# Kernel tuning notes

Hardware: AMD Instinct MI355X
Metric: run time of the kernel (lower is better)

Reference implementation:

```python
import jax, jax.numpy as jnp
import numpy as np

B, IN, H0, H1, OUT = 4096, 1024, 4096, 4096, 1024
QMAX = 127.0


def setup_inputs() -> dict:
    key = jax.random.key(0)
    k0, k1, k2, k3 = jax.random.split(key, 4)
    x = jax.random.normal(k0, (B, IN), dtype=jnp.float32)
    # Linear weights hold already-quantized integer values (module casts .int())
    W0 = jax.random.randint(k1, (H0, IN + 1), -127, 128).astype(jnp.int32)
    W1 = jax.random.randint(k2, (H1, H0 + 1), -127, 128).astype(jnp.int32)
    W2 = jax.random.randint(k3, (OUT, H1 + 1), -127, 128).astype(jnp.int32)
    return {
        "x": x,
        "a_in0": jnp.float32(4.0), "a_w0": jnp.float32(0.05),
        "a_in2": jnp.float32(50.0), "a_w2": jnp.float32(0.05),
        "a_in4": jnp.float32(50.0), "a_w4": jnp.float32(0.05),
        "W0": W0, "W1": W1, "W2": W2,
    }


def _quant(x, amax):
    # clamp(round(x * 127/amax), -127, 127) -> int32
    return jnp.clip(jnp.round(x * (QMAX / amax)), -QMAX, QMAX).astype(jnp.int32)


def _qlinear(x, W, a_in, a_w):
    q = _quant(x, a_in)                                   # [B, K] int32
    ones = jnp.ones((q.shape[0], 1), dtype=jnp.int32)     # folded bias column
    q = jnp.concatenate([q, ones], axis=1)                # [B, K+1]
    acc = q @ W.T                                         # int32 GEMM [B, N]
    return acc.astype(jnp.float32) * (a_w * a_in / (QMAX * QMAX))


def reference(x, a_in0, a_w0, a_in2, a_w2, a_in4, a_w4, W0, W1, W2):
    x = x.reshape(x.shape[0], -1)
    x = _qlinear(x, W0, a_in0, a_w0)
    x = jax.nn.relu(x)
    x = _qlinear(x, W1, a_in2, a_w2)
    x = jax.nn.relu(x)
    x = _qlinear(x, W2, a_in4, a_w4)
    return x
```

## Files before the change

### kernel.cpp

```cpp
#include <hip/hip_runtime.h>

#define QMAX 127.0f

typedef int v4i __attribute__((ext_vector_type(4)));

__device__ __forceinline__ void gload_lds16(const void* g, void* l) {
  __builtin_amdgcn_global_load_lds(
      (const __attribute__((address_space(1))) void*)g,
      (__attribute__((address_space(3))) void*)l, 16, 0, 0);
}

__device__ __forceinline__ void pack_body(const int* __restrict__ W,
                                          signed char* __restrict__ W8,
                                          int* __restrict__ bias,
                                          unsigned lblk, int kshift) {
  unsigned t = lblk * 256u + threadIdx.x;
  unsigned row = t >> kshift;
  unsigned j = t & ((1u << kshift) - 1u);
  unsigned K = 4u << kshift;
  size_t srcBase = (size_t)row * (size_t)(K + 1) + (size_t)j * 4;
  int c0 = W[srcBase + 0], c1 = W[srcBase + 1], c2 = W[srcBase + 2], c3 = W[srcBase + 3];
  unsigned packed = (unsigned)(c0 & 0xff) | ((unsigned)(c1 & 0xff) << 8) |
                    ((unsigned)(c2 & 0xff) << 16) | ((unsigned)(c3 & 0xff) << 24);
  reinterpret_cast<unsigned*>(W8)[t] = packed;
  if (j == 0) bias[row] = W[(size_t)row * (K + 1) + K];
}

__global__ void prep_kernel(const float* __restrict__ x,
                            signed char* __restrict__ qa0,
                            const float* __restrict__ pAin,
                            const int* __restrict__ W0, signed char* __restrict__ W0p, int* __restrict__ b0,
                            const int* __restrict__ W1, signed char* __restrict__ W1p, int* __restrict__ b1,
                            const int* __restrict__ W2, signed char* __restrict__ W2p, int* __restrict__ b2) {
  unsigned blk = blockIdx.x;
  if (blk < 4096u) {
    pack_body(W0, W0p, b0, blk, 8);
  } else if (blk < 20480u) {
    pack_body(W1, W1p, b1, blk - 4096u, 10);
  } else if (blk < 24576u) {
    pack_body(W2, W2p, b2, blk - 20480u, 10);
  } else {
    unsigned t = (blk - 24576u) * 256u + threadIdx.x;
    float s = QMAX / pAin[0];
    float4 v = reinterpret_cast<const float4*>(x)[t];
    int q0 = (int)fminf(fmaxf(rintf(v.x * s), -QMAX), QMAX);
    int q1 = (int)fminf(fmaxf(rintf(v.y * s), -QMAX), QMAX);
    int q2 = (int)fminf(fmaxf(rintf(v.z * s), -QMAX), QMAX);
    int q3 = (int)fminf(fmaxf(rintf(v.w * s), -QMAX), QMAX);
    unsigned packed = (unsigned)(q0 & 0xff) | ((unsigned)(q1 & 0xff) << 8) |
                      ((unsigned)(q2 & 0xff) << 16) | ((unsigned)(q3 & 0xff) << 24);
    reinterpret_cast<unsigned*>(qa0)[t] = packed;
  }
}


#define FENCE() asm volatile("" ::: "memory")
#define BARRIER()                      \
  do {                                 \
    FENCE();                           \
    __builtin_amdgcn_s_barrier();      \
    FENCE();                           \
  } while (0)
#define LGK0() asm volatile("s_waitcnt lgkmcnt(0)" ::: "memory")
#define VMC6() asm volatile("s_waitcnt vmcnt(6)" ::: "memory")
#define VMC0() asm volatile("s_waitcnt vmcnt(0)" ::: "memory")

#define STAGE_A(bf, h, t)                                                     \
  do {                                                                        \
    const signed char* _g = gA + (size_t)((h) * 128) * K + (size_t)(t) * 128; \
    signed char* _l = ldsA + (bf) * 32768 + (h) * 16384 + ldsThr;             \
    gload_lds16(_g, _l);                                                      \
    gload_lds16(_g + (size_t)8 * K, _l + 1024);                               \
  } while (0)

#define STAGE_B(bf, h, t)                                                     \
  do {                                                                        \
    const signed char* _g = gB + (size_t)((h) * 128) * K + (size_t)(t) * 128; \
    signed char* _l = ldsB + (bf) * 32768 + (h) * 16384 + ldsThr;             \
    gload_lds16(_g, _l);                                                      \
    gload_lds16(_g + (size_t)8 * K, _l + 1024);                               \
  } while (0)

#define LDAQ(bf, qm, kk, dst)                                                 \
  do {                                                                        \
    _Pragma("unroll") for (int m = 0; m < 4; ++m) {                           \
      int row = wm * 128 + (qm) * 64 + m * 16 + l15;                          \
      int off = ((kk) * 64 + hi * 16) ^ ((row & 7) << 4);                     \
      dst[m] = *(const v4i*)(ldsA + (bf) * 32768 + row * 128 + off);          \
    }                                                                         \
  } while (0)

#define LDBH(bf, kk)                                                          \
  do {                                                                        \
    _Pragma("unroll") for (int n = 0; n < 4; ++n) {                           \
      int row = wn * 64 + n * 16 + l15;                                       \
      int off = ((kk) * 64 + hi * 16) ^ ((row & 7) << 4);                     \
      bR[n][kk] = *(const v4i*)(ldsB + (bf) * 32768 + row * 128 + off);       \
    }                                                                         \
  } while (0)

#define MFMAQK(qm, kk, asrc)                                                  \
  do {                                                                        \
    __builtin_amdgcn_s_setprio(1);                                            \
    _Pragma("unroll") for (int m = 0; m < 4; ++m)                             \
    _Pragma("unroll") for (int n = 0; n < 4; ++n)                             \
      acc[(qm) * 4 + m][n] = __builtin_amdgcn_mfma_i32_16x16x64_i8(           \
          asrc[m], bR[n][kk], acc[(qm) * 4 + m][n], 0, 0, 0);                 \
    __builtin_amdgcn_s_setprio(0);                                            \
  } while (0)

__global__ __launch_bounds__(512, 2)
void qgemm256_kernel(const signed char* __restrict__ A,
                     const signed char* __restrict__ Bw,
                     const int* __restrict__ bias,
                     signed char* __restrict__ O,
                     int N, int K, int nbn,
                     const float* __restrict__ pAin,
                     const float* __restrict__ pAw,
                     const float* __restrict__ pAnext) {
  extern __shared__ signed char lds[];
  signed char* ldsA = lds;
  signed char* ldsB = lds + 65536;

  const int nwg = gridDim.x, bid = blockIdx.x, per = nwg >> 3;
  const int swz = (bid & 7) * per + (bid >> 3);
  const int brow = swz / nbn, bcol = swz - brow * nbn;
  const int browBase = brow << 8, bcolBase = bcol << 8;

  const int tid = threadIdx.x;
  const int lane = tid & 63, l15 = lane & 15, hi = lane >> 4;
  const int wid = tid >> 6, wm = wid >> 2, wn = wid & 3;

  const int rloc = (wid << 4) + (lane >> 3);
  const int csrc = (lane & 7) ^ ((lane >> 3) & 7);
  const signed char* gA = A + (size_t)(browBase + rloc) * K + csrc * 16;
  const signed char* gB = Bw + (size_t)(bcolBase + rloc) * K + csrc * 16;
  const int ldsThr = (wid << 11) + lane * 16;

  v4i acc[8][4] = {};
  v4i bR[4][2];

  const int nk = K >> 7, niter = nk >> 1, nkm = nk - 1;

  STAGE_B(0, 0, 0); STAGE_B(0, 1, 0); STAGE_A(0, 0, 0); STAGE_A(0, 1, 0);
  STAGE_B(1, 0, 1); STAGE_B(1, 1, 1); STAGE_A(1, 0, 1);
  VMC6();
  BARRIER();

#pragma unroll 1
  for (int i = 0; i < niter; ++i) {
    const int t1 = 2 * i + 1;
    const int tE = (2 * i + 2) & nkm;
    const int tO = (2 * i + 3) & nkm;
    v4i a00[4], a01[4], a10[4], a11[4];
    LDAQ(0, 0, 0, a00); LDBH(0, 0); LDAQ(0, 0, 1, a01); LDBH(0, 1);
    STAGE_A(1, 1, t1);
    BARRIER();
    MFMAQK(0, 0, a00);
    LGK0();
    BARRIER();
    LDAQ(0, 1, 0, a10);
    STAGE_B(0, 0, tE);
    BARRIER();
    MFMAQK(0, 1, a01);
    BARRIER();
    LDAQ(0, 1, 1, a11);
    STAGE_B(0, 1, tE);
    BARRIER();
    MFMAQK(1, 0, a10);
    LGK0();
    BARRIER();
    STAGE_A(0, 0, tE);
    VMC6();
    BARRIER();
    MFMAQK(1, 1, a11);
    BARRIER();
    LDAQ(1, 0, 0, a00); LDBH(1, 0); LDAQ(1, 0, 1, a01); LDBH(1, 1);
    STAGE_A(0, 1, tE);
    BARRIER();
    MFMAQK(0, 0, a00);
    LGK0();
    BARRIER();
    LDAQ(1, 1, 0, a10);
    STAGE_B(1, 0, tO);
    BARRIER();
    MFMAQK(0, 1, a01);
    BARRIER();
    LDAQ(1, 1, 1, a11);
    STAGE_B(1, 1, tO);
    BARRIER();
    MFMAQK(1, 0, a10);
    LGK0();
    BARRIER();
    STAGE_A(1, 0, tO);
    VMC6();
    BARRIER();
    MFMAQK(1, 1, a11);
    BARRIER();
  }

  VMC0();

  const float sDeq = (pAw[0] * pAin[0]) / (QMAX * QMAX);
  const float sQ = QMAX / pAnext[0];
#pragma unroll
  for (int nf = 0; nf < 4; ++nf) {
    const int gcol = bcolBase + wn * 64 + nf * 16 + l15;
    const int bv = bias[gcol];
#pragma unroll
    for (int mf = 0; mf < 8; ++mf) {
      const int gr = browBase + wm * 128 + mf * 16 + (hi << 2);
#pragma unroll
      for (int r = 0; r < 4; ++r) {
        float f = (float)(acc[mf][nf][r] + bv) * sDeq;
        f = fmaxf(f, 0.0f);
        float qf = fminf(fmaxf(rintf(f * sQ), -QMAX), QMAX);
        O[(size_t)(gr + r) * N + gcol] = (signed char)(int)qf;
      }
    }
  }
}

__global__ __launch_bounds__(256)
void qgemm_kernel(const signed char* __restrict__ A,
                  const signed char* __restrict__ Bw,
                  const int* __restrict__ bias,
                  float* __restrict__ O,
                  int N, int K, int nbn,
                  const float* __restrict__ pAin,
                  const float* __restrict__ pAw) {
  __shared__ signed char slds[32768];
  signed char* ldsA = slds;
  signed char* ldsB = slds + 16384;

  int nwg = gridDim.x;
  int bid = blockIdx.x;
  int per = nwg >> 3;
  int swz = (bid & 7) * per + (bid >> 3);
  int brow = swz / nbn;
  int bcol = swz - brow * nbn;
  int browBase = brow << 7;
  int bcolBase = bcol << 7;

  int tid = threadIdx.x;
  int lane = tid & 63;
  int l15 = lane & 15;
  int hi = lane >> 4;
  int wid = tid >> 6;
  int wr = (wid >> 1) << 6;
  int wc = (wid & 1) << 6;

  v4i acc[4][4] = {};

  int nk = K >> 7;
  for (int kt = 0; kt < nk; ++kt) {
    int k0 = kt << 7;
#pragma unroll
    for (int i = 0; i < 4; ++i) {
      int c = i * 256 + tid;
      int r = c >> 3;
      int osrc = ((c & 7) << 4) ^ ((r & 7) << 4);
      gload_lds16(A + (size_t)(browBase + r) * K + (k0 + osrc), ldsA + c * 16);
      gload_lds16(Bw + (size_t)(bcolBase + r) * K + (k0 + osrc), ldsB + c * 16);
    }
    __syncthreads();
#pragma unroll
    for (int kk = 0; kk < 2; ++kk) {
      v4i a[4], b[4];
#pragma unroll
      for (int m = 0; m < 4; ++m) {
        int row = wr + m * 16 + l15;
        int off = (kk * 64 + hi * 16) ^ ((row & 7) << 4);
        a[m] = *reinterpret_cast<const v4i*>(ldsA + row * 128 + off);
      }
#pragma unroll
      for (int n = 0; n < 4; ++n) {
        int row = wc + n * 16 + l15;
        int off = (kk * 64 + hi * 16) ^ ((row & 7) << 4);
        b[n] = *reinterpret_cast<const v4i*>(ldsB + row * 128 + off);
      }
#pragma unroll
      for (int m = 0; m < 4; ++m)
#pragma unroll
        for (int n = 0; n < 4; ++n)
          acc[m][n] = __builtin_amdgcn_mfma_i32_16x16x64_i8(a[m], b[n], acc[m][n], 0, 0, 0);
    }
    __syncthreads();
  }

  float sDeq = (pAw[0] * pAin[0]) / (QMAX * QMAX);
#pragma unroll
  for (int n = 0; n < 4; ++n) {
    int gcol = bcolBase + wc + n * 16 + l15;
    int bv = bias[gcol];
#pragma unroll
    for (int m = 0; m < 4; ++m) {
      int growb = browBase + wr + m * 16 + (hi << 2);
#pragma unroll
      for (int r = 0; r < 4; ++r) {
        O[(size_t)(growb + r) * N + gcol] = (float)(acc[m][n][r] + bv) * sDeq;
      }
    }
  }
}

extern "C" void kernel_launch(void* const* d_in, const int* in_sizes, int n_in,
                              void* d_out, int out_size, void* d_ws, size_t ws_size,
                              hipStream_t stream) {
  const float* x     = (const float*)d_in[0];
  const float* a_in0 = (const float*)d_in[1];
  const float* a_w0  = (const float*)d_in[2];
  const float* a_in2 = (const float*)d_in[3];
  const float* a_w2  = (const float*)d_in[4];
  const float* a_in4 = (const float*)d_in[5];
  const float* a_w4  = (const float*)d_in[6];
  const int*   W0    = (const int*)d_in[7];
  const int*   W1    = (const int*)d_in[8];
  const int*   W2    = (const int*)d_in[9];
  float* out = (float*)d_out;

  constexpr int B = 4096, IN = 1024, H0 = 4096, H1 = 4096, OUTN = 1024;

  char* ws = (char*)d_ws;
  size_t off = 0;
  auto alloc = [&](size_t sz) {
    char* p = ws + off;
    off += (sz + 255) & ~(size_t)255;
    return p;
  };
  signed char* qa0 = (signed char*)alloc((size_t)B * IN);
  signed char* qa1 = (signed char*)alloc((size_t)B * H0);
  signed char* qa2 = (signed char*)alloc((size_t)B * H1);
  signed char* W0p = (signed char*)alloc((size_t)H0 * IN);
  signed char* W1p = (signed char*)alloc((size_t)H1 * H0);
  signed char* W2p = (signed char*)alloc((size_t)OUTN * H1);
  int* b0 = (int*)alloc((size_t)H0 * 4);
  int* b1 = (int*)alloc((size_t)H1 * 4);
  int* b2 = (int*)alloc((size_t)OUTN * 4);

  hipFuncSetAttribute((const void*)qgemm256_kernel,
                      hipFuncAttributeMaxDynamicSharedMemorySize, 131072);

  prep_kernel<<<28672, 256, 0, stream>>>(x, qa0, a_in0,
                                         W0, W0p, b0,
                                         W1, W1p, b1,
                                         W2, W2p, b2);

  qgemm256_kernel<<<(B / 256) * (H0 / 256), 512, 131072, stream>>>(
      qa0, W0p, b0, qa1, H0, IN, H0 / 256, a_in0, a_w0, a_in2);

  qgemm256_kernel<<<(B / 256) * (H1 / 256), 512, 131072, stream>>>(
      qa1, W1p, b1, qa2, H1, H0, H1 / 256, a_in2, a_w2, a_in4);

  qgemm_kernel<<<(B / 128) * (OUTN / 128), 256, 0, stream>>>(
      qa2, W2p, b2, out, OUTN, H1, OUTN / 128, a_in4, a_w4);
}
```

Measured before the change: 141.5 us.

## Switch 256-tile int8 GEMM to 32x32x32 MFMA with prefetched LDS fragments

Replaces the 16x16x64 i8 MFMA tiles in the 256x256 kernel with 32x32x32 i8 MFMAs on a 4x2 fragment grid per wave. The K-loop is restructured so that LDS reads for the next 32-wide k-chunk are issued before the MFMAs of the current chunk, using ping-pong A registers. The goal is fewer LDS reads per MFMA and better overlap of LDS latency with matrix math. The cost is a more complex epilogue row mapping and higher register pressure from the 16-wide accumulators.

Measured after the change: 150.3 us. 1.06x slower.

```diff
diff --git a/kernel.cpp b/kernel.cpp
--- a/kernel.cpp
+++ b/kernel.cpp
@@ -3,6 +3,7 @@
 #define QMAX 127.0f
 
 typedef int v4i __attribute__((ext_vector_type(4)));
+typedef int v16i __attribute__((ext_vector_type(16)));
 
 __device__ __forceinline__ void gload_lds16(const void* g, void* l) {
   __builtin_amdgcn_global_load_lds(
@@ -81,31 +82,31 @@
     gload_lds16(_g + (size_t)8 * K, _l + 1024);                               \
   } while (0)
 
-#define LDAQ(bf, qm, kk, dst)                                                 \
-  do {                                                                        \
-    _Pragma("unroll") for (int m = 0; m < 4; ++m) {                           \
-      int row = wm * 128 + (qm) * 64 + m * 16 + l15;                          \
-      int off = ((kk) * 64 + hi * 16) ^ ((row & 7) << 4);                     \
-      dst[m] = *(const v4i*)(ldsA + (bf) * 32768 + row * 128 + off);          \
+#define LDA4(bf, kc, dst)                                                     \
+  do {                                                                        \
+    _Pragma("unroll") for (int mf = 0; mf < 4; ++mf) {                        \
+      int row = wm * 128 + mf * 32 + l31;                                     \
+      int off = ((kc) * 32 + hk * 16) ^ ((row & 7) << 4);                     \
+      dst[mf] = *(const v4i*)(ldsA + (bf) * 32768 + row * 128 + off);         \
     }                                                                         \
   } while (0)
 
-#define LDBH(bf, kk)                                                          \
-  do {                                                                        \
-    _Pragma("unroll") for (int n = 0; n < 4; ++n) {                           \
-      int row = wn * 64 + n * 16 + l15;                                       \
-      int off = ((kk) * 64 + hi * 16) ^ ((row & 7) << 4);                     \
-      bR[n][kk] = *(const v4i*)(ldsB + (bf) * 32768 + row * 128 + off);       \
+#define LDB2(bf, kc)                                                          \
+  do {                                                                        \
+    _Pragma("unroll") for (int nf = 0; nf < 2; ++nf) {                        \
+      int row = wn * 64 + nf * 32 + l31;                                      \
+      int off = ((kc) * 32 + hk * 16) ^ ((row & 7) << 4);                     \
+      bF[nf][kc] = *(const v4i*)(ldsB + (bf) * 32768 + row * 128 + off);      \
     }                                                                         \
   } while (0)
 
-#define MFMAQK(qm, kk, asrc)                                                  \
+#define MFMA8(aset, kc)                                                       \
   do {                                                                        \
     __builtin_amdgcn_s_setprio(1);                                            \
-    _Pragma("unroll") for (int m = 0; m < 4; ++m)                             \
-    _Pragma("unroll") for (int n = 0; n < 4; ++n)                             \
-      acc[(qm) * 4 + m][n] = __builtin_amdgcn_mfma_i32_16x16x64_i8(           \
-          asrc[m], bR[n][kk], acc[(qm) * 4 + m][n], 0, 0, 0);                 \
+    _Pragma("unroll") for (int mf = 0; mf < 4; ++mf)                          \
+    _Pragma("unroll") for (int nf = 0; nf < 2; ++nf)                          \
+      acc[mf][nf] = __builtin_amdgcn_mfma_i32_32x32x32_i8(                    \
+          aset[mf], bF[nf][kc], acc[mf][nf], 0, 0, 0);                        \
     __builtin_amdgcn_s_setprio(0);                                            \
   } while (0)
 
@@ -128,7 +129,7 @@
   const int browBase = brow << 8, bcolBase = bcol << 8;
 
   const int tid = threadIdx.x;
-  const int lane = tid & 63, l15 = lane & 15, hi = lane >> 4;
+  const int lane = tid & 63, l31 = lane & 31, hk = lane >> 5;
   const int wid = tid >> 6, wm = wid >> 2, wn = wid & 3;
 
   const int rloc = (wid << 4) + (lane >> 3);
@@ -137,8 +138,8 @@
   const signed char* gB = Bw + (size_t)(bcolBase + rloc) * K + csrc * 16;
   const int ldsThr = (wid << 11) + lane * 16;
 
-  v4i acc[8][4] = {};
-  v4i bR[4][2];
+  v16i acc[4][2] = {};
+  v4i aP[4], aQ[4], bF[2][4];
 
   const int nk = K >> 7, niter = nk >> 1, nkm = nk - 1;
 
@@ -146,56 +147,59 @@
   STAGE_B(1, 0, 1); STAGE_B(1, 1, 1); STAGE_A(1, 0, 1);
   VMC6();
   BARRIER();
+  LDA4(0, 0, aP);
+  LDB2(0, 0); LDB2(0, 1);
 
 #pragma unroll 1
   for (int i = 0; i < niter; ++i) {
     const int t1 = 2 * i + 1;
     const int tE = (2 * i + 2) & nkm;
     const int tO = (2 * i + 3) & nkm;
-    v4i a00[4], a01[4], a10[4], a11[4];
-    LDAQ(0, 0, 0, a00); LDBH(0, 0); LDAQ(0, 0, 1, a01); LDBH(0, 1);
     STAGE_A(1, 1, t1);
     BARRIER();
-    MFMAQK(0, 0, a00);
+    LDA4(0, 1, aQ); LDB2(0, 2); LDB2(0, 3);
+    MFMA8(aP, 0);
     LGK0();
     BARRIER();
-    LDAQ(0, 1, 0, a10);
     STAGE_B(0, 0, tE);
     BARRIER();
-    MFMAQK(0, 1, a01);
-    BARRIER();
-    LDAQ(0, 1, 1, a11);
+    LDA4(0, 2, aP);
+    MFMA8(aQ, 1);
+    BARRIER();
     STAGE_B(0, 1, tE);
     BARRIER();
-    MFMAQK(1, 0, a10);
+    LDA4(0, 3, aQ);
+    MFMA8(aP, 2);
     LGK0();
     BARRIER();
     STAGE_A(0, 0, tE);
     VMC6();
     BARRIER();
-    MFMAQK(1, 1, a11);
-    BARRIER();
-    LDAQ(1, 0, 0, a00); LDBH(1, 0); LDAQ(1, 0, 1, a01); LDBH(1, 1);
+    LDA4(1, 0, aP); LDB2(1, 0); LDB2(1, 1);
+    MFMA8(aQ, 3);
+    BARRIER();
     STAGE_A(0, 1, tE);
     BARRIER();
-    MFMAQK(0, 0, a00);
+    LDA4(1, 1, aQ); LDB2(1, 2); LDB2(1, 3);
+    MFMA8(aP, 0);
     LGK0();
     BARRIER();
-    LDAQ(1, 1, 0, a10);
     STAGE_B(1, 0, tO);
     BARRIER();
-    MFMAQK(0, 1, a01);
-    BARRIER();
-    LDAQ(1, 1, 1, a11);
+    LDA4(1, 2, aP);
+    MFMA8(aQ, 1);
+    BARRIER();
     STAGE_B(1, 1, tO);
     BARRIER();
-    MFMAQK(1, 0, a10);
+    LDA4(1, 3, aQ);
+    MFMA8(aP, 2);
     LGK0();
     BARRIER();
     STAGE_A(1, 0, tO);
     VMC6();
     BARRIER();
-    MFMAQK(1, 1, a11);
+    LDA4(0, 0, aP); LDB2(0, 0); LDB2(0, 1);
+    MFMA8(aQ, 3);
     BARRIER();
   }
 
@@ -204,18 +208,19 @@
   const float sDeq = (pAw[0] * pAin[0]) / (QMAX * QMAX);
   const float sQ = QMAX / pAnext[0];
 #pragma unroll
-  for (int nf = 0; nf < 4; ++nf) {
-    const int gcol = bcolBase + wn * 64 + nf * 16 + l15;
+  for (int nf = 0; nf < 2; ++nf) {
+    const int gcol = bcolBase + wn * 64 + nf * 32 + l31;
     const int bv = bias[gcol];
 #pragma unroll
-    for (int mf = 0; mf < 8; ++mf) {
-      const int gr = browBase + wm * 128 + mf * 16 + (hi << 2);
-#pragma unroll
-      for (int r = 0; r < 4; ++r) {
+    for (int mf = 0; mf < 4; ++mf) {
+      const int growB = browBase + wm * 128 + mf * 32 + 4 * hk;
+#pragma unroll
+      for (int r = 0; r < 16; ++r) {
+        const int grow = growB + (r & 3) + 8 * (r >> 2);
         float f = (float)(acc[mf][nf][r] + bv) * sDeq;
         f = fmaxf(f, 0.0f);
         float qf = fminf(fmaxf(rintf(f * sQ), -QMAX), QMAX);
-        O[(size_t)(gr + r) * N + gcol] = (signed char)(int)qf;
+        O[(size_t)grow * N + gcol] = (signed char)(int)qf;
       }
     }
   }
```

## Restructure int8 GEMM main loop into coarser stages with fewer barriers

Applied to the files above, without the earlier changes.

Reworks the software pipeline of the 256x256 int8 MFMA GEMM main loop. Each half-tile now loads both K sub-steps of A and B fragments at once and issues 32 MFMAs per phase, instead of 16 per quarter-step. The global-to-LDS staging order changes so that A halves are issued together, and the wait becomes vmcnt(8). This cuts the number of barriers and waitcnts per iteration, which the change intends to reduce sync overhead. In exchange it gives up the finer interleaving of LDS reads with MFMA and raises register pressure from holding all A fragments at once.

Result: no change. 142.9 us (+1.0%).

```diff
diff --git a/kernel.cpp b/kernel.cpp
--- a/kernel.cpp
+++ b/kernel.cpp
@@ -62,7 +62,7 @@
     FENCE();                           \
   } while (0)
 #define LGK0() asm volatile("s_waitcnt lgkmcnt(0)" ::: "memory")
-#define VMC6() asm volatile("s_waitcnt vmcnt(6)" ::: "memory")
+#define VMC8() asm volatile("s_waitcnt vmcnt(8)" ::: "memory")
 #define VMC0() asm volatile("s_waitcnt vmcnt(0)" ::: "memory")
 
 #define STAGE_A(bf, h, t)                                                     \
@@ -81,31 +81,36 @@
     gload_lds16(_g + (size_t)8 * K, _l + 1024);                               \
   } while (0)
 
-#define LDAQ(bf, qm, kk, dst)                                                 \
+#define LDAQ(bf, qm)                                                          \
   do {                                                                        \
     _Pragma("unroll") for (int m = 0; m < 4; ++m) {                           \
       int row = wm * 128 + (qm) * 64 + m * 16 + l15;                          \
-      int off = ((kk) * 64 + hi * 16) ^ ((row & 7) << 4);                     \
-      dst[m] = *(const v4i*)(ldsA + (bf) * 32768 + row * 128 + off);          \
+      _Pragma("unroll") for (int kk = 0; kk < 2; ++kk) {                      \
+        int off = (kk * 64 + hi * 16) ^ ((row & 7) << 4);                     \
+        aq[m][kk] = *(const v4i*)(ldsA + (bf) * 32768 + row * 128 + off);     \
+      }                                                                       \
     }                                                                         \
   } while (0)
 
-#define LDBH(bf, kk)                                                          \
+#define LDBF(bf)                                                              \
   do {                                                                        \
     _Pragma("unroll") for (int n = 0; n < 4; ++n) {                           \
       int row = wn * 64 + n * 16 + l15;                                       \
-      int off = ((kk) * 64 + hi * 16) ^ ((row & 7) << 4);                     \
-      bR[n][kk] = *(const v4i*)(ldsB + (bf) * 32768 + row * 128 + off);       \
+      _Pragma("unroll") for (int kk = 0; kk < 2; ++kk) {                      \
+        int off = (kk * 64 + hi * 16) ^ ((row & 7) << 4);                     \
+        bR[n][kk] = *(const v4i*)(ldsB + (bf) * 32768 + row * 128 + off);     \
+      }                                                                       \
     }                                                                         \
   } while (0)
 
-#define MFMAQK(qm, kk, asrc)                                                  \
+#define MFMAC(qm)                                                             \
   do {                                                                        \
     __builtin_amdgcn_s_setprio(1);                                            \
     _Pragma("unroll") for (int m = 0; m < 4; ++m)                             \
     _Pragma("unroll") for (int n = 0; n < 4; ++n)                             \
+    _Pragma("unroll") for (int kk = 0; kk < 2; ++kk)                          \
       acc[(qm) * 4 + m][n] = __builtin_amdgcn_mfma_i32_16x16x64_i8(           \
-          asrc[m], bR[n][kk], acc[(qm) * 4 + m][n], 0, 0, 0);                 \
+          aq[m][kk], bR[n][kk], acc[(qm) * 4 + m][n], 0, 0, 0);               \
     __builtin_amdgcn_s_setprio(0);                                            \
   } while (0)
 
@@ -143,59 +148,37 @@
   const int nk = K >> 7, niter = nk >> 1, nkm = nk - 1;
 
   STAGE_B(0, 0, 0); STAGE_B(0, 1, 0); STAGE_A(0, 0, 0); STAGE_A(0, 1, 0);
-  STAGE_B(1, 0, 1); STAGE_B(1, 1, 1); STAGE_A(1, 0, 1);
-  VMC6();
-  BARRIER();
+  STAGE_B(1, 0, 1); STAGE_B(1, 1, 1);
 
 #pragma unroll 1
   for (int i = 0; i < niter; ++i) {
     const int t1 = 2 * i + 1;
     const int tE = (2 * i + 2) & nkm;
     const int tO = (2 * i + 3) & nkm;
-    v4i a00[4], a01[4], a10[4], a11[4];
-    LDAQ(0, 0, 0, a00); LDBH(0, 0); LDAQ(0, 0, 1, a01); LDBH(0, 1);
-    STAGE_A(1, 1, t1);
-    BARRIER();
-    MFMAQK(0, 0, a00);
+    v4i aq[4][2];
+    STAGE_A(1, 0, t1); STAGE_A(1, 1, t1);
+    VMC8();
+    BARRIER();
+    LDAQ(0, 0); LDBF(0);
+    MFMAC(0);
     LGK0();
     BARRIER();
-    LDAQ(0, 1, 0, a10);
-    STAGE_B(0, 0, tE);
-    BARRIER();
-    MFMAQK(0, 1, a01);
-    BARRIER();
-    LDAQ(0, 1, 1, a11);
-    STAGE_B(0, 1, tE);
-    BARRIER();
-    MFMAQK(1, 0, a10);
+    STAGE_B(0, 0, tE); STAGE_B(0, 1, tE);
+    LDAQ(0, 1);
+    MFMAC(1);
     LGK0();
     BARRIER();
-    STAGE_A(0, 0, tE);
-    VMC6();
-    BARRIER();
-    MFMAQK(1, 1, a11);
-    BARRIER();
-    LDAQ(1, 0, 0, a00); LDBH(1, 0); LDAQ(1, 0, 1, a01); LDBH(1, 1);
-    STAGE_A(0, 1, tE);
-    BARRIER();
-    MFMAQK(0, 0, a00);
+    STAGE_A(0, 0, tE); STAGE_A(0, 1, tE);
+    VMC8();
+    BARRIER();
+    LDAQ(1, 0); LDBF(1);
+    MFMAC(0);
     LGK0();
     BARRIER();
-    LDAQ(1, 1, 0, a10);
-    STAGE_B(1, 0, tO);
-    BARRIER();
-    MFMAQK(0, 1, a01);
-    BARRIER();
-    LDAQ(1, 1, 1, a11);
-    STAGE_B(1, 1, tO);
-    BARRIER();
-    MFMAQK(1, 0, a10);
+    STAGE_B(1, 0, tO); STAGE_B(1, 1, tO);
+    LDAQ(1, 1);
+    MFMAC(1);
     LGK0();
-    BARRIER();
-    STAGE_A(1, 0, tO);
-    VMC6();
-    BARRIER();
-    MFMAQK(1, 1, a11);
     BARRIER();
   }
 
```
